# Optimization experiments

Measured on AMD Instinct MI355X. Metric: run time of the kernel, lower is better.

## Reference

```python
import jax, jax.numpy as jnp
import numpy as np

EMBED_DIM = 1024
NUM_HEADS = 16
HEAD_DIM = EMBED_DIM // NUM_HEADS


def setup_inputs() -> dict:
    key = jax.random.key(0)
    ks = jax.random.split(key, 11)
    B, T, D = 4, 2048, EMBED_DIM
    s = 1.0 / np.sqrt(D)
    inp = {
        "x": jax.random.normal(ks[0], (B, T, D), dtype=jnp.float32),
        "wq": jax.random.normal(ks[1], (D, D), dtype=jnp.float32) * s,
        "bq": jnp.zeros((D,), dtype=jnp.float32),
        "wk": jax.random.normal(ks[2], (D, D), dtype=jnp.float32) * s,
        "bk": jnp.zeros((D,), dtype=jnp.float32),
        "wv": jax.random.normal(ks[3], (D, D), dtype=jnp.float32) * s,
        "bv": jnp.zeros((D,), dtype=jnp.float32),
        "wo": jax.random.normal(ks[4], (D, D), dtype=jnp.float32) * s,
        "bo": jnp.zeros((D,), dtype=jnp.float32),
        "ln_gamma": jnp.ones((D,), dtype=jnp.float32),
        "ln_beta": jnp.zeros((D,), dtype=jnp.float32),
    }
    return inp


def _attention(x, wq, bq, wk, bk, wv, bv, wo, bo, ln_gamma, ln_beta):
    B, T, D = x.shape
    H, Hd = NUM_HEADS, HEAD_DIM
    # projections -> (B, H, T, Hd)
    q = (x @ wq + bq).reshape(B, T, H, Hd).transpose(0, 2, 1, 3)
    k = (x @ wk + bk).reshape(B, T, H, Hd).transpose(0, 2, 1, 3)
    v = (x @ wv + bv).reshape(B, T, H, Hd).transpose(0, 2, 1, 3)
    scores = jnp.einsum("bhqd,bhkd->bhqk", q, k) / jnp.sqrt(jnp.asarray(Hd, x.dtype))
    attn = jax.nn.softmax(scores, axis=-1)  # dropout p=0 -> identity
    out = jnp.einsum("bhqk,bhkd->bhqd", attn, v)
    out = out.transpose(0, 2, 1, 3).reshape(B, T, D)
    out = out @ wo + bo
    # LayerNorm (no residual in the original forward)
    mu = jnp.mean(out, axis=-1, keepdims=True)
    var = jnp.var(out, axis=-1, keepdims=True)
    out = (out - mu) / jnp.sqrt(var + 1e-5) * ln_gamma + ln_beta
    return out


def reference(x, wq, bq, wk, bk, wv, bv, wo, bo, ln_gamma, ln_beta):
    return _attention(x, wq, bq, wk, bk, wv, bv, wo, bo, ln_gamma, ln_beta)
```

## Files before the change

kernel.cpp:

```cpp
#include <hip/hip_runtime.h>
#include <hip/hip_bf16.h>

typedef __bf16 bf16_t;
typedef __bf16 bf16x4v __attribute__((ext_vector_type(4)));
typedef __bf16 bf16x8 __attribute__((ext_vector_type(8)));
typedef float  f32x4  __attribute__((ext_vector_type(4)));

typedef __attribute__((address_space(1))) void* gptr_t;
typedef __attribute__((address_space(3))) void* lptr_t;

#define B_BATCH  4
#define T_SEQ    2048
#define D_MODEL  1024
#define N_HEADS  16
#define HEAD_DIM 64
#define M_ROWS   (B_BATCH * T_SEQ)

#define BM  128
#define BN  128
#define BKK 64
#define PROW 40
#define CPAD 136

#define EXP2_SCALE 0.1803368801111204f

__global__ __launch_bounds__(256) void cvt_x(
    const float* __restrict__ in, bf16_t* __restrict__ out)
{
    const size_t i = ((size_t)blockIdx.x * 256 + threadIdx.x) * 4;
    const f32x4 v = *(const f32x4*)&in[i];
    bf16x4v o;
    for (int e = 0; e < 4; e++) o[e] = (bf16_t)v[e];
    *(bf16x4v*)&out[i] = o;
}

__global__ __launch_bounds__(256) void transpose_w(
    const float* __restrict__ w0, const float* __restrict__ w1,
    const float* __restrict__ w2, const float* __restrict__ w3,
    bf16_t* __restrict__ out)
{
    __shared__ bf16_t tile[32][33];
    const int z = blockIdx.z;
    const float* w = (z == 0) ? w0 : (z == 1) ? w1 : (z == 2) ? w2 : w3;
    bf16_t* o = out + (size_t)z * D_MODEL * D_MODEL;
    const int tx = threadIdx.x & 31, ty = threadIdx.x >> 5;
    const int k0 = blockIdx.y * 32, n0 = blockIdx.x * 32;
    for (int i = 0; i < 4; i++)
        tile[ty + i * 8][tx] = (bf16_t)w[(size_t)(k0 + ty + i * 8) * D_MODEL + n0 + tx];
    __syncthreads();
    for (int i = 0; i < 4; i++)
        o[(size_t)(n0 + ty + i * 8) * D_MODEL + k0 + tx] = tile[tx][ty + i * 8];
}

template <int MODE>
__global__ __launch_bounds__(256) void gemm_k(
    const bf16_t* __restrict__ A, const bf16_t* __restrict__ wT_base,
    const float* __restrict__ b0, const float* __restrict__ b1,
    const float* __restrict__ b2,
    void* __restrict__ out_base, void* __restrict__ out2)
{
    __shared__ __attribute__((aligned(16))) bf16_t smem[17408];
    bf16_t (*As)[BKK]  = reinterpret_cast<bf16_t(*)[BKK]>(&smem[0]);
    bf16_t (*Bs)[BKK]  = reinterpret_cast<bf16_t(*)[BKK]>(&smem[8192]);
    bf16_t (*Cs)[CPAD] = reinterpret_cast<bf16_t(*)[CPAD]>(&smem[0]);

    const int tid  = threadIdx.x;
    const int z    = blockIdx.z;
    const bf16_t* BT   = wT_base + (size_t)z * D_MODEL * D_MODEL;
    const float*  bias = (MODE == 1) ? b0 : ((z == 0) ? b0 : (z == 1) ? b1 : b2);
    const int mbase = blockIdx.y * BM;
    const int nbase = blockIdx.x * BN;
    const int w = tid >> 6, lane = tid & 63, quad = lane >> 4, l16 = lane & 15;
    const int wm = (w & 1) * 64, wn = (w >> 1) * 64;
    const int lrow = lane >> 3, lcol = (lane & 7) * 8;

    f32x4 acc[4][4] = {};

    for (int kb = 0; kb < D_MODEL; kb += BKK) {
        __syncthreads();
        for (int it = 0; it < 4; it++) {
            const int r = w * 32 + it * 8;
            __builtin_amdgcn_global_load_lds(
                (gptr_t)&A [(size_t)(mbase + r + lrow) * D_MODEL + kb + lcol],
                (lptr_t)&As[r][0], 16, 0, 0);
            __builtin_amdgcn_global_load_lds(
                (gptr_t)&BT[(size_t)(nbase + r + lrow) * D_MODEL + kb + lcol],
                (lptr_t)&Bs[r][0], 16, 0, 0);
        }
        __syncthreads();
        for (int s = 0; s < 2; s++) {
            bf16x8 af[4], bf[4];
            for (int i = 0; i < 4; i++)
                af[i] = *(const bf16x8*)&As[wm + i * 16 + l16][s * 32 + quad * 8];
            for (int j = 0; j < 4; j++)
                bf[j] = *(const bf16x8*)&Bs[wn + j * 16 + l16][s * 32 + quad * 8];
            for (int i = 0; i < 4; i++)
                for (int j = 0; j < 4; j++)
                    acc[i][j] = __builtin_amdgcn_mfma_f32_16x16x32_bf16(
                        af[i], bf[j], acc[i][j], 0, 0, 0);
        }
    }

    float bj[4];
    for (int j = 0; j < 4; j++)
        bj[j] = bias[nbase + wn + j * 16 + l16];

    if (MODE == 1) {
        for (int i = 0; i < 4; i++)
            for (int r = 0; r < 4; r++) {
                const int rg = mbase + wm + i * 16 + quad * 4 + r;
                for (int j = 0; j < 4; j++) {
                    const int cg = nbase + wn + j * 16 + l16;
                    ((float*)out_base)[(size_t)rg * D_MODEL + cg] = acc[i][j][r] + bj[j];
                }
            }
    } else {
        const int vmode = (z == 2);
        __syncthreads();
        for (int i = 0; i < 4; i++)
            for (int r = 0; r < 4; r++) {
                const int row = wm + i * 16 + quad * 4 + r;
                for (int j = 0; j < 4; j++) {
                    const int col = wn + j * 16 + l16;
                    const float v = acc[i][j][r] + bj[j];
                    if (!vmode) Cs[row][col] = (bf16_t)v;
                    else        Cs[col][row] = (bf16_t)v;
                }
            }
        __syncthreads();

        const int bidx  = mbase >> 11;
        const int t0    = mbase & 2047;
        const int hbase = nbase >> 6;
        for (int p = 0; p < 8; p++) {
            const int chunk = p * 256 + tid;
            if (!vmode) {
                const int sub = chunk & 7, run = chunk >> 3;
                const int t = run & 127, hl = run >> 7;
                const bf16x8 val = *(const bf16x8*)&Cs[t][hl * 64 + sub * 8];
                bf16_t* q = (bf16_t*)out_base + (size_t)z * ((size_t)M_ROWS * D_MODEL);
                *(bf16x8*)&q[(((size_t)(bidx * N_HEADS + hbase + hl)) * T_SEQ + t0 + t)
                             * HEAD_DIM + sub * 8] = val;
            } else {
                const int sub = chunk & 15, hdl = chunk >> 4;
                const int h = hbase + (hdl >> 6), hd = hdl & 63;
                const bf16x8 val = *(const bf16x8*)&Cs[hdl][sub * 8];
                *(bf16x8*)&((bf16_t*)out2)[(((size_t)(bidx * N_HEADS + h)) * HEAD_DIM + hd)
                                           * T_SEQ + t0 + sub * 8] = val;
            }
        }
    }
}

__global__ __launch_bounds__(256, 4) void attn_k(
    const bf16_t* __restrict__ Q, const bf16_t* __restrict__ K,
    const bf16_t* __restrict__ VT, bf16_t* __restrict__ O)
{
    __shared__ __attribute__((aligned(16))) bf16_t Ks[2][64 * 64];
    __shared__ __attribute__((aligned(16))) bf16_t Vs[64 * 64];
    __shared__ __attribute__((aligned(16))) bf16_t Ps[4][32][PROW];

    const int tid = threadIdx.x;
    const int f = blockIdx.y * 16 + blockIdx.x;
    const int xcd = f & 7, j = f >> 3;
    const int bh = xcd * 8 + (j & 7);
    const int qbase = (j >> 3) * 128;
    const int b = bh >> 4, h = bh & 15;
    const int w = tid >> 6, lane = tid & 63, quad = lane >> 4, l16 = lane & 15;
    const size_t head_off = (size_t)bh * T_SEQ * HEAD_DIM;
    const bf16_t* Qh  = Q  + head_off;
    const bf16_t* Kh  = K  + head_off;
    const bf16_t* VTh = VT + head_off;

    const int srow = lane >> 3;
    const int scol = ((lane & 7) ^ srow) * 8;

    const int rxor = l16 & 7;
    const int rc0 = ((0 + quad) ^ rxor) * 8;
    const int rc1 = ((4 + quad) ^ rxor) * 8;

    bf16x8 bq[2][2];
    for (int iq = 0; iq < 2; iq++)
        for (int s = 0; s < 2; s++)
            bq[iq][s] = *(const bf16x8*)
                &Qh[(size_t)(qbase + w * 32 + iq * 16 + l16) * HEAD_DIM + s * 32 + quad * 8];

    for (int it = 0; it < 2; it++) {
        const int R = w * 16 + it * 8;
        __builtin_amdgcn_global_load_lds(
            (gptr_t)&Kh[(size_t)(R + srow) * HEAD_DIM + scol],
            (lptr_t)&Ks[0][R * 64], 16, 0, 0);
    }

    float l_part[2] = {0.f, 0.f};
    f32x4 Oacc[2][4] = {};

    for (int kt = 0; kt < T_SEQ / 64; kt++) {
        const int kbase = kt * 64;
        __syncthreads();
        const bf16_t* Kc = Ks[kt & 1];

        for (int it = 0; it < 2; it++) {
            const int R = w * 16 + it * 8;
            __builtin_amdgcn_global_load_lds(
                (gptr_t)&VTh[(size_t)(R + srow) * T_SEQ + kbase + scol],
                (lptr_t)&Vs[R * 64], 16, 0, 0);
        }
        if (kt + 1 < T_SEQ / 64) {
            bf16_t* Kn = Ks[(kt + 1) & 1];
            for (int it = 0; it < 2; it++) {
                const int R = w * 16 + it * 8;
                __builtin_amdgcn_global_load_lds(
                    (gptr_t)&Kh[(size_t)(kbase + 64 + R + srow) * HEAD_DIM + scol],
                    (lptr_t)&Kn[R * 64], 16, 0, 0);
            }
        }

        f32x4 St[4][2] = {};
        for (int s = 0; s < 2; s++) {
            const int rc = s ? rc1 : rc0;
            bf16x8 ak[4];
            for (int jk = 0; jk < 4; jk++)
                ak[jk] = *(const bf16x8*)&Kc[(jk * 16 + l16) * 64 + rc];
            __builtin_amdgcn_s_setprio(1);
            for (int jk = 0; jk < 4; jk++)
                for (int iq = 0; iq < 2; iq++)
                    St[jk][iq] = __builtin_amdgcn_mfma_f32_16x16x32_bf16(
                        ak[jk], bq[iq][s], St[jk][iq], 0, 0, 0);
            __builtin_amdgcn_s_setprio(0);
        }

        for (int kk = 0; kk < 2; kk++)
            for (int iq = 0; iq < 2; iq++) {
                bf16x4v pv;
                for (int r = 0; r < 4; r++) {
                    const float p = __builtin_amdgcn_exp2f(St[kk][iq][r] * EXP2_SCALE);
                    l_part[iq] += p;
                    pv[r] = (bf16_t)p;
                }
                *(bf16x4v*)&Ps[w][iq * 16 + l16][kk * 16 + quad * 4] = pv;
            }
        asm volatile("" ::: "memory");

        __syncthreads();

        {
            bf16x8 ap[2], bv[4];
            for (int iq = 0; iq < 2; iq++)
                ap[iq] = *(const bf16x8*)&Ps[w][iq * 16 + l16][quad * 8];
            for (int jn = 0; jn < 4; jn++)
                bv[jn] = *(const bf16x8*)&Vs[(jn * 16 + l16) * 64 + rc0];
            __builtin_amdgcn_s_setprio(1);
            for (int iq = 0; iq < 2; iq++)
                for (int jn = 0; jn < 4; jn++)
                    Oacc[iq][jn] = __builtin_amdgcn_mfma_f32_16x16x32_bf16(
                        ap[iq], bv[jn], Oacc[iq][jn], 0, 0, 0);
            __builtin_amdgcn_s_setprio(0);
        }

        for (int kk = 0; kk < 2; kk++)
            for (int iq = 0; iq < 2; iq++) {
                bf16x4v pv;
                for (int r = 0; r < 4; r++) {
                    const float p = __builtin_amdgcn_exp2f(St[2 + kk][iq][r] * EXP2_SCALE);
                    l_part[iq] += p;
                    pv[r] = (bf16_t)p;
                }
                *(bf16x4v*)&Ps[w][iq * 16 + l16][kk * 16 + quad * 4] = pv;
            }
        asm volatile("" ::: "memory");

        {
            bf16x8 ap[2], bv[4];
            for (int iq = 0; iq < 2; iq++)
                ap[iq] = *(const bf16x8*)&Ps[w][iq * 16 + l16][quad * 8];
            for (int jn = 0; jn < 4; jn++)
                bv[jn] = *(const bf16x8*)&Vs[(jn * 16 + l16) * 64 + rc1];
            __builtin_amdgcn_s_setprio(1);
            for (int iq = 0; iq < 2; iq++)
                for (int jn = 0; jn < 4; jn++)
                    Oacc[iq][jn] = __builtin_amdgcn_mfma_f32_16x16x32_bf16(
                        ap[iq], bv[jn], Oacc[iq][jn], 0, 0, 0);
            __builtin_amdgcn_s_setprio(0);
        }
    }

    for (int iq = 0; iq < 2; iq++) {
        l_part[iq] += __shfl_xor(l_part[iq], 16, 64);
        l_part[iq] += __shfl_xor(l_part[iq], 32, 64);
    }

    for (int iq = 0; iq < 2; iq++) {
        for (int r = 0; r < 4; r++) {
            const int qrow = quad * 4 + r;
            const float inv = 1.f / __shfl(l_part[iq], qrow, 64);
            const int t = qbase + w * 32 + iq * 16 + qrow;
            for (int jn = 0; jn < 4; jn++) {
                const int hd = jn * 16 + l16;
                O[(((size_t)(b * T_SEQ + t)) * N_HEADS + h) * HEAD_DIM + hd] =
                    (bf16_t)(Oacc[iq][jn][r] * inv);
            }
        }
    }
}

__global__ __launch_bounds__(256) void ln_k(
    const float* __restrict__ proj, const float* __restrict__ gamma,
    const float* __restrict__ beta, float* __restrict__ out)
{
    __shared__ float red[4][2];
    const int row = blockIdx.x, tid = threadIdx.x;
    const float* p = proj + (size_t)row * D_MODEL + tid * 4;
    const f32x4 v = *(const f32x4*)p;
    float s1 = v[0] + v[1] + v[2] + v[3];
    float s2 = v[0] * v[0] + v[1] * v[1] + v[2] * v[2] + v[3] * v[3];
    for (int off = 32; off >= 1; off >>= 1) {
        s1 += __shfl_xor(s1, off, 64);
        s2 += __shfl_xor(s2, off, 64);
    }
    const int w = tid >> 6;
    if ((tid & 63) == 0) { red[w][0] = s1; red[w][1] = s2; }
    __syncthreads();
    const float S1 = red[0][0] + red[1][0] + red[2][0] + red[3][0];
    const float S2 = red[0][1] + red[1][1] + red[2][1] + red[3][1];
    const float mu  = S1 * (1.f / D_MODEL);
    const float var = S2 * (1.f / D_MODEL) - mu * mu;
    const float rstd = rsqrtf(var + 1e-5f);
    const int c = tid * 4;
    f32x4 o;
    for (int e = 0; e < 4; e++)
        o[e] = (v[e] - mu) * rstd * gamma[c + e] + beta[c + e];
    *(f32x4*)&out[(size_t)row * D_MODEL + c] = o;
}

extern "C" void kernel_launch(void* const* d_in, const int* in_sizes, int n_in,
                              void* d_out, int out_size, void* d_ws, size_t ws_size,
                              hipStream_t stream)
{
    const float* x  = (const float*)d_in[0];
    const float* wq = (const float*)d_in[1];
    const float* bq = (const float*)d_in[2];
    const float* wk = (const float*)d_in[3];
    const float* bk = (const float*)d_in[4];
    const float* wv = (const float*)d_in[5];
    const float* bv = (const float*)d_in[6];
    const float* wo = (const float*)d_in[7];
    const float* bo = (const float*)d_in[8];
    const float* g  = (const float*)d_in[9];
    const float* be = (const float*)d_in[10];

    char* ws = (char*)d_ws;
    bf16_t* xb   = (bf16_t*)(ws);
    bf16_t* wT   = (bf16_t*)(ws + ((size_t)16 << 20));
    bf16_t* qkv  = (bf16_t*)(ws + ((size_t)24 << 20));
    bf16_t* attn = (bf16_t*)(ws + ((size_t)72 << 20));
    float*  proj = (float*) (ws + ((size_t)88 << 20));
    bf16_t* vt   = (bf16_t*)proj;

    cvt_x<<<dim3(M_ROWS * D_MODEL / 1024), 256, 0, stream>>>(x, xb);
    transpose_w<<<dim3(32, 32, 4), 256, 0, stream>>>(wq, wk, wv, wo, wT);

    gemm_k<3><<<dim3(8, 64, 3), 256, 0, stream>>>(
        xb, wT, bq, bk, bv, (void*)qkv, (void*)vt);

    bf16_t* Qm = qkv;
    bf16_t* Km = qkv + (size_t)M_ROWS * D_MODEL;

    attn_k<<<dim3(16, 64), 256, 0, stream>>>(Qm, Km, vt, attn);

    gemm_k<1><<<dim3(8, 64, 1), 256, 0, stream>>>(
        attn, wT + (size_t)3 * D_MODEL * D_MODEL, bo, bo, bo, (void*)proj, nullptr);

    ln_k<<<dim3(M_ROWS), 256, 0, stream>>>(proj, g, be, (float*)d_out);
}
```

Baseline: 318.1 us.

## Load GEMM B operand directly from global, widen cvt and LayerNorm per-thread work

The GEMM kernel no longer stages the weight tile in LDS. Each wave loads its B fragments straight from global memory into registers, so only A goes through LDS. The x-conversion kernel now handles four vectors per thread with a quarter of the blocks. LayerNorm assigns one wave per row, which removes the LDS reduction and the block barrier, and loads gamma and beta as vectors. Direct global B loads lose the reuse that LDS gave across waves and may add latency that is not hidden in the GEMM inner loop.

```diff
diff --git a/kernel.cpp b/kernel.cpp
--- a/kernel.cpp
+++ b/kernel.cpp
@@ -27,11 +27,14 @@
 __global__ __launch_bounds__(256) void cvt_x(
     const float* __restrict__ in, bf16_t* __restrict__ out)
 {
-    const size_t i = ((size_t)blockIdx.x * 256 + threadIdx.x) * 4;
-    const f32x4 v = *(const f32x4*)&in[i];
-    bf16x4v o;
-    for (int e = 0; e < 4; e++) o[e] = (bf16_t)v[e];
-    *(bf16x4v*)&out[i] = o;
+    const size_t tid = (size_t)blockIdx.x * 256 + threadIdx.x;
+    for (int rep = 0; rep < 4; rep++) {
+        const size_t i = (tid + (size_t)rep * 524288) * 4;
+        const f32x4 v = *(const f32x4*)&in[i];
+        bf16x4v o;
+        for (int e = 0; e < 4; e++) o[e] = (bf16_t)v[e];
+        *(bf16x4v*)&out[i] = o;
+    }
 }
 
 __global__ __launch_bounds__(256) void transpose_w(
@@ -61,7 +64,6 @@
 {
     __shared__ __attribute__((aligned(16))) bf16_t smem[17408];
     bf16_t (*As)[BKK]  = reinterpret_cast<bf16_t(*)[BKK]>(&smem[0]);
-    bf16_t (*Bs)[BKK]  = reinterpret_cast<bf16_t(*)[BKK]>(&smem[8192]);
     bf16_t (*Cs)[CPAD] = reinterpret_cast<bf16_t(*)[CPAD]>(&smem[0]);
 
     const int tid  = threadIdx.x;
@@ -74,6 +76,10 @@
     const int wm = (w & 1) * 64, wn = (w >> 1) * 64;
     const int lrow = lane >> 3, lcol = (lane & 7) * 8;
 
+    const bf16_t* Bl[4];
+    for (int j = 0; j < 4; j++)
+        Bl[j] = BT + (size_t)(nbase + wn + j * 16 + l16) * D_MODEL + quad * 8;
+
     f32x4 acc[4][4] = {};
 
     for (int kb = 0; kb < D_MODEL; kb += BKK) {
@@ -81,23 +87,22 @@
         for (int it = 0; it < 4; it++) {
             const int r = w * 32 + it * 8;
             __builtin_amdgcn_global_load_lds(
-                (gptr_t)&A [(size_t)(mbase + r + lrow) * D_MODEL + kb + lcol],
+                (gptr_t)&A[(size_t)(mbase + r + lrow) * D_MODEL + kb + lcol],
                 (lptr_t)&As[r][0], 16, 0, 0);
-            __builtin_amdgcn_global_load_lds(
-                (gptr_t)&BT[(size_t)(nbase + r + lrow) * D_MODEL + kb + lcol],
-                (lptr_t)&Bs[r][0], 16, 0, 0);
-        }
+        }
+        bf16x8 bf[2][4];
+        for (int s = 0; s < 2; s++)
+            for (int j = 0; j < 4; j++)
+                bf[s][j] = *(const bf16x8*)&Bl[j][kb + s * 32];
         __syncthreads();
         for (int s = 0; s < 2; s++) {
-            bf16x8 af[4], bf[4];
+            bf16x8 af[4];
             for (int i = 0; i < 4; i++)
                 af[i] = *(const bf16x8*)&As[wm + i * 16 + l16][s * 32 + quad * 8];
-            for (int j = 0; j < 4; j++)
-                bf[j] = *(const bf16x8*)&Bs[wn + j * 16 + l16][s * 32 + quad * 8];
             for (int i = 0; i < 4; i++)
                 for (int j = 0; j < 4; j++)
                     acc[i][j] = __builtin_amdgcn_mfma_f32_16x16x32_bf16(
-                        af[i], bf[j], acc[i][j], 0, 0, 0);
+                        af[i], bf[s][j], acc[i][j], 0, 0, 0);
         }
     }
 
@@ -308,29 +313,32 @@
     const float* __restrict__ proj, const float* __restrict__ gamma,
     const float* __restrict__ beta, float* __restrict__ out)
 {
-    __shared__ float red[4][2];
-    const int row = blockIdx.x, tid = threadIdx.x;
-    const float* p = proj + (size_t)row * D_MODEL + tid * 4;
-    const f32x4 v = *(const f32x4*)p;
-    float s1 = v[0] + v[1] + v[2] + v[3];
-    float s2 = v[0] * v[0] + v[1] * v[1] + v[2] * v[2] + v[3] * v[3];
+    const int tid = threadIdx.x;
+    const int w = tid >> 6, lane = tid & 63;
+    const int row = blockIdx.x * 4 + w;
+    const float* p = proj + (size_t)row * D_MODEL;
+    f32x4 v[4];
+    float s1 = 0.f, s2 = 0.f;
+    for (int e = 0; e < 4; e++) {
+        v[e] = *(const f32x4*)&p[e * 256 + lane * 4];
+        for (int k = 0; k < 4; k++) { s1 += v[e][k]; s2 += v[e][k] * v[e][k]; }
+    }
     for (int off = 32; off >= 1; off >>= 1) {
         s1 += __shfl_xor(s1, off, 64);
         s2 += __shfl_xor(s2, off, 64);
     }
-    const int w = tid >> 6;
-    if ((tid & 63) == 0) { red[w][0] = s1; red[w][1] = s2; }
-    __syncthreads();
-    const float S1 = red[0][0] + red[1][0] + red[2][0] + red[3][0];
-    const float S2 = red[0][1] + red[1][1] + red[2][1] + red[3][1];
-    const float mu  = S1 * (1.f / D_MODEL);
-    const float var = S2 * (1.f / D_MODEL) - mu * mu;
+    const float mu  = s1 * (1.f / D_MODEL);
+    const float var = s2 * (1.f / D_MODEL) - mu * mu;
     const float rstd = rsqrtf(var + 1e-5f);
-    const int c = tid * 4;
-    f32x4 o;
-    for (int e = 0; e < 4; e++)
-        o[e] = (v[e] - mu) * rstd * gamma[c + e] + beta[c + e];
-    *(f32x4*)&out[(size_t)row * D_MODEL + c] = o;
+    float* o = out + (size_t)row * D_MODEL;
+    for (int e = 0; e < 4; e++) {
+        const int c = e * 256 + lane * 4;
+        const f32x4 g4 = *(const f32x4*)&gamma[c];
+        const f32x4 b4 = *(const f32x4*)&beta[c];
+        f32x4 ov;
+        for (int k = 0; k < 4; k++) ov[k] = (v[e][k] - mu) * rstd * g4[k] + b4[k];
+        *(f32x4*)&o[c] = ov;
+    }
 }
 
 extern "C" void kernel_launch(void* const* d_in, const int* in_sizes, int n_in,
@@ -357,7 +365,7 @@
     float*  proj = (float*) (ws + ((size_t)88 << 20));
     bf16_t* vt   = (bf16_t*)proj;
 
-    cvt_x<<<dim3(M_ROWS * D_MODEL / 1024), 256, 0, stream>>>(x, xb);
+    cvt_x<<<dim3(2048), 256, 0, stream>>>(x, xb);
     transpose_w<<<dim3(32, 32, 4), 256, 0, stream>>>(wq, wk, wv, wo, wT);
 
     gemm_k<3><<<dim3(8, 64, 3), 256, 0, stream>>>(
@@ -371,5 +379,5 @@
     gemm_k<1><<<dim3(8, 64, 1), 256, 0, stream>>>(
         attn, wT + (size_t)3 * D_MODEL * D_MODEL, bo, bo, bo, (void*)proj, nullptr);
 
-    ln_k<<<dim3(M_ROWS), 256, 0, stream>>>(proj, g, be, (float*)d_out);
-}
+    ln_k<<<dim3(M_ROWS / 4), 256, 0, stream>>>(proj, g, be, (float*)d_out);
+}
```

Result: slower. 352.5 us (+10.8%).
